# Performance work log

Measured on AMD Instinct MI355X. Metric: run time of the kernel, lower is better.

The kernel has to match this reference:

```python
import jax, jax.numpy as jnp
import numpy as np

NU = 100000  # num 'user' nodes
NI = 100000  # num 'item' nodes
E = 600000   # edges per relation
IN_DIM = 128
HID = 128
OUT = 64


def setup_inputs() -> dict:
    key = jax.random.key(0)
    ks = jax.random.split(key, 14)
    return {
        "x_user": jax.random.normal(ks[0], (NU, IN_DIM), jnp.float32),
        "x_item": jax.random.normal(ks[1], (NI, IN_DIM), jnp.float32),
        "W_proj": jax.random.normal(ks[2], (IN_DIM, HID), jnp.float32) / np.sqrt(IN_DIM),
        "b_proj": jax.random.normal(ks[3], (HID,), jnp.float32) * 0.01,
        "W_out": jax.random.normal(ks[4], (HID, OUT), jnp.float32) / np.sqrt(HID),
        "b_out": jax.random.normal(ks[5], (OUT,), jnp.float32) * 0.01,
        "al1": jax.random.normal(ks[6], (1,), jnp.float32),
        "ar1": jax.random.normal(ks[7], (1,), jnp.float32),
        "al2": jax.random.normal(ks[8], (1,), jnp.float32),
        "ar2": jax.random.normal(ks[9], (1,), jnp.float32),
        "e1_src": jax.random.randint(ks[10], (E,), 0, NU, jnp.int32),  # user->user
        "e1_dst": jax.random.randint(ks[11], (E,), 0, NU, jnp.int32),
        "e2_src": jax.random.randint(ks[12], (E,), 0, NI, jnp.int32),  # item->user
        "e2_dst": jax.random.randint(ks[13], (E,), 0, NU, jnp.int32),
    }


def reference(x_user, x_item, W_proj, b_proj, W_out, b_out,
              al1, ar1, al2, ar2, e1_src, e1_dst, e2_src, e2_dst):
    # Shared projection for every node type
    h_user = x_user @ W_proj + b_proj  # [NU, HID]
    h_item = x_item @ W_proj + b_proj  # [NI, HID]

    # Relation ('user','u2u','user'): msg = h_src*al + h_dst*ar, scatter-add to dst
    msg1 = h_user[e1_src] * al1 + h_user[e1_dst] * ar1  # [E, HID]
    out_user = jax.ops.segment_sum(msg1, e1_dst, num_segments=NU)

    # Relation ('item','i2u','user')
    msg2 = h_item[e2_src] * al2 + h_user[e2_dst] * ar2  # [E, HID]
    out_user = out_user + jax.ops.segment_sum(msg2, e2_dst, num_segments=NU)

    # 'item' receives no messages -> zeros
    out_item = jnp.zeros_like(h_item)

    out_user = jax.nn.elu(out_user)
    out_item = jax.nn.elu(out_item)

    # out_layer applied only to 'user'
    out_user = out_user @ W_out + b_out  # [NU, OUT]
    return out_user, out_item
```

## Files before the change

kernel.cpp:

```cpp
#include <hip/hip_runtime.h>
#include <hip/hip_bf16.h>
#include <math.h>

#define NUSER 100000
#define NITEM 100000
#define NEDGE 600000
#define HID   128
#define OUTD  64
#define LDA   136
#define LDF   132
#define PROJ_BLOCKS ((NUSER + NITEM) / 64)
#define EPB   ((2 * NEDGE + PROJ_BLOCKS - 1) / PROJ_BLOCKS)

typedef __attribute__((ext_vector_type(8))) short  bf16x8;
typedef __attribute__((ext_vector_type(4))) float  f32x4;
typedef __attribute__((ext_vector_type(4))) unsigned short u16x4;

__device__ inline unsigned short f2bf(float f) {
    __hip_bfloat16 h = __float2bfloat16(f);
    return *reinterpret_cast<unsigned short*>(&h);
}

__device__ inline void bf2x(unsigned int u, float& lo, float& hi) {
    union { unsigned int i; float f; } a, b;
    a.i = u << 16;
    b.i = u & 0xffff0000u;
    lo = a.f; hi = b.f;
}

__global__ void prep(const float* __restrict__ W, unsigned short* __restrict__ wt,
                     int* __restrict__ deg) {
    int i = blockIdx.x * 256 + threadIdx.x;
    if (i < 2 * NUSER) deg[i] = 0;
    if (i < 128 * 128) {
        int k = i >> 7, c = i & 127;
        wt[c * 128 + k] = f2bf(W[i]);
    }
}

__global__ void count_rank(const int* __restrict__ e1d, const int* __restrict__ e2d,
                           int* __restrict__ deg1, int* __restrict__ deg2,
                           int* __restrict__ rank) {
    int i = blockIdx.x * blockDim.x + threadIdx.x;
    if (i < NEDGE)            rank[i] = atomicAdd(&deg1[e1d[i]], 1);
    else if (i < 2 * NEDGE)   rank[i] = atomicAdd(&deg2[e2d[i - NEDGE]], 1);
}

#define SCAN_BLOCKS 391

__global__ __launch_bounds__(256) void scanA(
    const int* __restrict__ deg1, const int* __restrict__ deg2,
    int* __restrict__ off, int* __restrict__ bsum)
{
    __shared__ int sh[256];
    int t = threadIdx.x;
    int i = blockIdx.x * 256 + t;
    int d = (i < NUSER) ? deg1[i] + deg2[i] : 0;
    sh[t] = d;
    __syncthreads();
    for (int dd = 1; dd < 256; dd <<= 1) {
        int v = (t >= dd) ? sh[t - dd] : 0;
        __syncthreads();
        sh[t] += v;
        __syncthreads();
    }
    if (i < NUSER) off[i] = (t > 0) ? sh[t - 1] : 0;
    if (t == 255) bsum[blockIdx.x] = sh[255];
}

__global__ __launch_bounds__(512) void scanB(int* __restrict__ bsum, int* __restrict__ off) {
    __shared__ int sh[512];
    int t = threadIdx.x;
    int v = (t < SCAN_BLOCKS) ? bsum[t] : 0;
    sh[t] = v;
    __syncthreads();
    for (int dd = 1; dd < 512; dd <<= 1) {
        int x = (t >= dd) ? sh[t - dd] : 0;
        __syncthreads();
        sh[t] += x;
        __syncthreads();
    }
    if (t < SCAN_BLOCKS) bsum[t] = (t > 0) ? sh[t - 1] : 0;
    if (t == 511) off[NUSER] = sh[511];
}

__global__ __launch_bounds__(256) void scanC(int* __restrict__ off, const int* __restrict__ bsum) {
    int i = blockIdx.x * 256 + threadIdx.x;
    if (i < NUSER) off[i] += bsum[blockIdx.x];
}

__global__ __launch_bounds__(256) void proj_fill(
    const float* __restrict__ xu, const float* __restrict__ xi,
    const unsigned short* __restrict__ wt, const float* __restrict__ b,
    unsigned short* __restrict__ h,
    const int* __restrict__ e1s, const int* __restrict__ e1d,
    const int* __restrict__ e2s, const int* __restrict__ e2d,
    const int* __restrict__ off, const int* __restrict__ deg1,
    const int* __restrict__ rank, int* __restrict__ adj)
{
    __shared__ unsigned short Wl[128 * LDA];
    __shared__ unsigned short Al[64 * LDA];
    const int tid = threadIdx.x;
    const int r0  = blockIdx.x * 64;

    for (int i = tid; i < 2048; i += 256) {
        int col = i >> 4, kc = i & 15;
        *(bf16x8*)&Wl[col * LDA + kc * 8] = *(const bf16x8*)&wt[col * 128 + kc * 8];
    }
    for (int i = tid; i < 2048; i += 256) {
        int row = i >> 5, c4 = i & 31;
        int gr = r0 + row;
        const float4* src = (gr < NUSER)
            ? (const float4*)(xu + (size_t)gr * 128)
            : (const float4*)(xi + (size_t)(gr - NUSER) * 128);
        float4 v = src[c4];
        u16x4 p;
        p.x = f2bf(v.x); p.y = f2bf(v.y); p.z = f2bf(v.z); p.w = f2bf(v.w);
        *(u16x4*)&Al[row * LDA + c4 * 4] = p;
    }
    __syncthreads();

    const int w    = tid >> 6;
    const int lane = tid & 63;
    const int lrow = lane & 15;
    const int lk   = (lane >> 4) * 8;

    f32x4 acc[4][2] = {};

    #pragma unroll
    for (int kc = 0; kc < 4; kc++) {
        const int ko = kc * 32 + lk;
        bf16x8 b0 = *(const bf16x8*)&Wl[(w * 32 + lrow) * LDA + ko];
        bf16x8 b1 = *(const bf16x8*)&Wl[(w * 32 + 16 + lrow) * LDA + ko];
        #pragma unroll
        for (int rt = 0; rt < 4; rt++) {
            bf16x8 aa = *(const bf16x8*)&Al[(rt * 16 + lrow) * LDA + ko];
            acc[rt][0] = __builtin_amdgcn_mfma_f32_16x16x32_bf16(aa, b0, acc[rt][0], 0, 0, 0);
            acc[rt][1] = __builtin_amdgcn_mfma_f32_16x16x32_bf16(aa, b1, acc[rt][1], 0, 0, 0);
        }
    }

    const float bv0 = b[w * 32 + lrow];
    const float bv1 = b[w * 32 + 16 + lrow];
    #pragma unroll
    for (int rt = 0; rt < 4; rt++) {
        #pragma unroll
        for (int ct = 0; ct < 2; ct++) {
            int col = w * 32 + ct * 16 + lrow;
            float bv = ct ? bv1 : bv0;
            #pragma unroll
            for (int r = 0; r < 4; r++) {
                int row = r0 + rt * 16 + (lane >> 4) * 4 + r;
                h[(size_t)row * 128 + col] = f2bf(acc[rt][ct][r] + bv);
            }
        }
    }

    const int base = blockIdx.x * EPB;
    const int lim  = (base + EPB < 2 * NEDGE) ? base + EPB : 2 * NEDGE;
    for (int i = base + tid; i < lim; i += 256) {
        int src, dst, slot;
        if (i < NEDGE) {
            src  = e1s[i];
            dst  = e1d[i];
            slot = off[dst] + rank[i];
        } else {
            int j = i - NEDGE;
            src  = NUSER + e2s[j];
            dst  = e2d[j];
            slot = off[dst] + deg1[dst] + rank[i];
        }
        adj[slot] = src;
    }
}

__global__ __launch_bounds__(256) void gather(
    const unsigned short* __restrict__ h, const int* __restrict__ adj,
    const int* __restrict__ off, const int* __restrict__ deg1,
    const int* __restrict__ deg2,
    const float* __restrict__ al1p, const float* __restrict__ ar1p,
    const float* __restrict__ al2p, const float* __restrict__ ar2p,
    float* __restrict__ acc)
{
    int wid  = (int)((blockIdx.x * 256 + threadIdx.x) >> 6);
    int lane = threadIdx.x & 63;
    if (wid >= NUSER) return;

    const unsigned int* h32 = (const unsigned int*)h;

    const float al1 = al1p[0], al2 = al2p[0];
    const float sc  = ar1p[0] * (float)deg1[wid] + ar2p[0] * (float)deg2[wid];

    float lo, hi;
    bf2x(h32[(size_t)wid * 64 + lane], lo, hi);
    float sx = sc * lo, sy = sc * hi;

    int e    = off[wid];
    int eend = off[wid + 1];
    for (; e + 4 <= eend; e += 4) {
        int s0 = adj[e], s1 = adj[e + 1], s2 = adj[e + 2], s3 = adj[e + 3];
        unsigned int u0 = h32[(size_t)s0 * 64 + lane];
        unsigned int u1 = h32[(size_t)s1 * 64 + lane];
        unsigned int u2 = h32[(size_t)s2 * 64 + lane];
        unsigned int u3 = h32[(size_t)s3 * 64 + lane];
        float a0 = (s0 < NUSER) ? al1 : al2;
        float a1 = (s1 < NUSER) ? al1 : al2;
        float a2 = (s2 < NUSER) ? al1 : al2;
        float a3 = (s3 < NUSER) ? al1 : al2;
        float x0, y0, x1, y1, x2, y2, x3, y3;
        bf2x(u0, x0, y0); bf2x(u1, x1, y1); bf2x(u2, x2, y2); bf2x(u3, x3, y3);
        sx = fmaf(a0, x0, sx); sy = fmaf(a0, y0, sy);
        sx = fmaf(a1, x1, sx); sy = fmaf(a1, y1, sy);
        sx = fmaf(a2, x2, sx); sy = fmaf(a2, y2, sy);
        sx = fmaf(a3, x3, sx); sy = fmaf(a3, y3, sy);
    }
    for (; e < eend; e++) {
        int s0 = adj[e];
        float a0 = (s0 < NUSER) ? al1 : al2;
        float x0, y0;
        bf2x(h32[(size_t)s0 * 64 + lane], x0, y0);
        sx = fmaf(a0, x0, sx); sy = fmaf(a0, y0, sy);
    }

    sx = sx > 0.f ? sx : expm1f(sx);
    sy = sy > 0.f ? sy : expm1f(sy);
    ((float2*)(acc + (size_t)wid * 128))[lane] = make_float2(sx, sy);
}

__global__ __launch_bounds__(256) void finalize(
    const float* __restrict__ acc, const float* __restrict__ Wo,
    const float* __restrict__ bo, float* __restrict__ out,
    float* __restrict__ accw)
{
    __shared__ float Wl[128 * 64];
    __shared__ float Al[64 * LDF];
    const int tid = threadIdx.x;
    const int n0  = blockIdx.x * 64;

    for (int i = tid; i < 128 * 64 / 4; i += 256)
        ((float4*)Wl)[i] = ((const float4*)Wo)[i];

    for (int i = tid; i < 2048; i += 256) {
        int row = i >> 5, c4 = i & 31;
        int gr = n0 + row;
        float4 v = (gr < NUSER) ? ((const float4*)(acc + (size_t)gr * 128))[c4]
                                : make_float4(0.f, 0.f, 0.f, 0.f);
        *(float4*)&Al[row * LDF + c4 * 4] = v;
    }
    __syncthreads();

    for (int i = tid; i < 2048; i += 256) {
        int row = i >> 5, c4 = i & 31;
        int gr = n0 + row;
        if (gr < NUSER)
            ((float4*)(accw + (size_t)gr * 128))[c4] = make_float4(0.f, 0.f, 0.f, 0.f);
    }

    const int tr = tid >> 4;
    const int tc = tid & 15;

    float s[4][4];
    {
        float4 bv = *(const float4*)&bo[tc * 4];
        #pragma unroll
        for (int i = 0; i < 4; i++) {
            s[i][0] = bv.x; s[i][1] = bv.y; s[i][2] = bv.z; s[i][3] = bv.w;
        }
    }

    for (int k0 = 0; k0 < 128; k0 += 4) {
        float4 av[4];
        #pragma unroll
        for (int i = 0; i < 4; i++)
            av[i] = *(const float4*)&Al[(tr * 4 + i) * LDF + k0];
        #pragma unroll
        for (int kk = 0; kk < 4; kk++) {
            float4 wv = *(const float4*)&Wl[(k0 + kk) * 64 + tc * 4];
            #pragma unroll
            for (int i = 0; i < 4; i++) {
                float a = (&av[i].x)[kk];
                s[i][0] = fmaf(a, wv.x, s[i][0]);
                s[i][1] = fmaf(a, wv.y, s[i][1]);
                s[i][2] = fmaf(a, wv.z, s[i][2]);
                s[i][3] = fmaf(a, wv.w, s[i][3]);
            }
        }
    }

    #pragma unroll
    for (int i = 0; i < 4; i++) {
        int gr = n0 + tr * 4 + i;
        if (gr < NUSER) {
            float4 o = make_float4(s[i][0], s[i][1], s[i][2], s[i][3]);
            *(float4*)&out[(size_t)gr * 64 + tc * 4] = o;
        }
    }
}

extern "C" void kernel_launch(void* const* d_in, const int* in_sizes, int n_in,
                              void* d_out, int out_size, void* d_ws, size_t ws_size,
                              hipStream_t stream) {
    const float* xu  = (const float*)d_in[0];
    const float* xi  = (const float*)d_in[1];
    const float* Wp  = (const float*)d_in[2];
    const float* bp  = (const float*)d_in[3];
    const float* Wo  = (const float*)d_in[4];
    const float* bo  = (const float*)d_in[5];
    const float* al1 = (const float*)d_in[6];
    const float* ar1 = (const float*)d_in[7];
    const float* al2 = (const float*)d_in[8];
    const float* ar2 = (const float*)d_in[9];
    const int* e1s = (const int*)d_in[10];
    const int* e1d = (const int*)d_in[11];
    const int* e2s = (const int*)d_in[12];
    const int* e2d = (const int*)d_in[13];

    float* out = (float*)d_out;
    float* acc = out + (size_t)NUSER * OUTD;

    unsigned short* h  = (unsigned short*)d_ws;
    unsigned short* wt = h + (size_t)(NUSER + NITEM) * HID;

    int* meta = (int*)out;
    int* deg1 = meta;
    int* deg2 = meta + NUSER;
    int* off  = meta + 2 * NUSER;
    int* bsum = meta + 3 * NUSER + 64;
    int* adj  = meta + 3 * NUSER + 1024;
    int* rank = adj + 2 * NEDGE;

    prep<<<(2 * NUSER + 255) / 256, 256, 0, stream>>>(Wp, wt, deg1);

    count_rank<<<(2 * NEDGE + 255) / 256, 256, 0, stream>>>(e1d, e2d, deg1, deg2, rank);

    scanA<<<SCAN_BLOCKS, 256, 0, stream>>>(deg1, deg2, off, bsum);
    scanB<<<1, 512, 0, stream>>>(bsum, off);
    scanC<<<SCAN_BLOCKS, 256, 0, stream>>>(off, bsum);

    proj_fill<<<PROJ_BLOCKS, 256, 0, stream>>>(xu, xi, wt, bp, h,
                                               e1s, e1d, e2s, e2d,
                                               off, deg1, rank, adj);

    gather<<<(NUSER * 64) / 256, 256, 0, stream>>>(h, adj, off, deg1, deg2,
                                                   al1, ar1, al2, ar2, acc);

    finalize<<<(NUSER + 63) / 64, 256, 0, stream>>>(acc, Wo, bo, out, acc);
}
```

Measured before the change: 213.8 us.

## Stage projection output through LDS, read weights from global, store activations as bf16

The projection kernel no longer copies the weight matrix into shared memory and reads B fragments straight from global/L2. Its output tile is staged through the freed LDS buffer so h is written with coalesced 16-byte stores instead of scattered 2-byte stores. The gather kernel now writes post-ELU activations as packed bf16 into a workspace buffer rather than fp32 into the output region, halving that intermediate's traffic. The cost is extra precision loss on the activations and repeated uncached-in-LDS weight reads per wave.

```diff
diff --git a/kernel.cpp b/kernel.cpp
--- a/kernel.cpp
+++ b/kernel.cpp
@@ -98,15 +98,10 @@
     const int* __restrict__ off, const int* __restrict__ deg1,
     const int* __restrict__ rank, int* __restrict__ adj)
 {
-    __shared__ unsigned short Wl[128 * LDA];
     __shared__ unsigned short Al[64 * LDA];
     const int tid = threadIdx.x;
     const int r0  = blockIdx.x * 64;
 
-    for (int i = tid; i < 2048; i += 256) {
-        int col = i >> 4, kc = i & 15;
-        *(bf16x8*)&Wl[col * LDA + kc * 8] = *(const bf16x8*)&wt[col * 128 + kc * 8];
-    }
     for (int i = tid; i < 2048; i += 256) {
         int row = i >> 5, c4 = i & 31;
         int gr = r0 + row;
@@ -130,8 +125,8 @@
     #pragma unroll
     for (int kc = 0; kc < 4; kc++) {
         const int ko = kc * 32 + lk;
-        bf16x8 b0 = *(const bf16x8*)&Wl[(w * 32 + lrow) * LDA + ko];
-        bf16x8 b1 = *(const bf16x8*)&Wl[(w * 32 + 16 + lrow) * LDA + ko];
+        bf16x8 b0 = *(const bf16x8*)&wt[(size_t)(w * 32 + lrow) * 128 + ko];
+        bf16x8 b1 = *(const bf16x8*)&wt[(size_t)(w * 32 + 16 + lrow) * 128 + ko];
         #pragma unroll
         for (int rt = 0; rt < 4; rt++) {
             bf16x8 aa = *(const bf16x8*)&Al[(rt * 16 + lrow) * LDA + ko];
@@ -140,6 +135,7 @@
         }
     }
 
+    __syncthreads();
     const float bv0 = b[w * 32 + lrow];
     const float bv1 = b[w * 32 + 16 + lrow];
     #pragma unroll
@@ -150,10 +146,17 @@
             float bv = ct ? bv1 : bv0;
             #pragma unroll
             for (int r = 0; r < 4; r++) {
-                int row = r0 + rt * 16 + (lane >> 4) * 4 + r;
-                h[(size_t)row * 128 + col] = f2bf(acc[rt][ct][r] + bv);
+                int row = rt * 16 + (lane >> 4) * 4 + r;
+                Al[row * LDA + col] = f2bf(acc[rt][ct][r] + bv);
             }
         }
+    }
+    __syncthreads();
+
+    for (int i = tid; i < 1024; i += 256) {
+        int row = i >> 4, c8 = i & 15;
+        *(bf16x8*)&h[(size_t)(r0 + row) * 128 + c8 * 8] =
+            *(const bf16x8*)&Al[row * LDA + c8 * 8];
     }
 
     const int base = blockIdx.x * EPB;
@@ -180,7 +183,7 @@
     const int* __restrict__ deg2,
     const float* __restrict__ al1p, const float* __restrict__ ar1p,
     const float* __restrict__ al2p, const float* __restrict__ ar2p,
-    float* __restrict__ acc)
+    unsigned int* __restrict__ accb)
 {
     int wid  = (int)((blockIdx.x * 256 + threadIdx.x) >> 6);
     int lane = threadIdx.x & 63;
@@ -224,13 +227,14 @@
 
     sx = sx > 0.f ? sx : expm1f(sx);
     sy = sy > 0.f ? sy : expm1f(sy);
-    ((float2*)(acc + (size_t)wid * 128))[lane] = make_float2(sx, sy);
+    unsigned int pk = ((unsigned int)f2bf(sy) << 16) | (unsigned int)f2bf(sx);
+    accb[(size_t)wid * 64 + lane] = pk;
 }
 
 __global__ __launch_bounds__(256) void finalize(
-    const float* __restrict__ acc, const float* __restrict__ Wo,
+    const unsigned int* __restrict__ accb, const float* __restrict__ Wo,
     const float* __restrict__ bo, float* __restrict__ out,
-    float* __restrict__ accw)
+    float* __restrict__ oitem)
 {
     __shared__ float Wl[128 * 64];
     __shared__ float Al[64 * LDF];
@@ -240,12 +244,12 @@
     for (int i = tid; i < 128 * 64 / 4; i += 256)
         ((float4*)Wl)[i] = ((const float4*)Wo)[i];
 
-    for (int i = tid; i < 2048; i += 256) {
-        int row = i >> 5, c4 = i & 31;
+    for (int i = tid; i < 4096; i += 256) {
+        int row = i >> 6, d = i & 63;
         int gr = n0 + row;
-        float4 v = (gr < NUSER) ? ((const float4*)(acc + (size_t)gr * 128))[c4]
-                                : make_float4(0.f, 0.f, 0.f, 0.f);
-        *(float4*)&Al[row * LDF + c4 * 4] = v;
+        float lo = 0.f, hi = 0.f;
+        if (gr < NUSER) bf2x(accb[(size_t)gr * 64 + d], lo, hi);
+        *(float2*)&Al[row * LDF + d * 2] = make_float2(lo, hi);
     }
     __syncthreads();
 
@@ -253,7 +257,7 @@
         int row = i >> 5, c4 = i & 31;
         int gr = n0 + row;
         if (gr < NUSER)
-            ((float4*)(accw + (size_t)gr * 128))[c4] = make_float4(0.f, 0.f, 0.f, 0.f);
+            ((float4*)(oitem + (size_t)gr * 128))[c4] = make_float4(0.f, 0.f, 0.f, 0.f);
     }
 
     const int tr = tid >> 4;
@@ -315,11 +319,12 @@
     const int* e2s = (const int*)d_in[12];
     const int* e2d = (const int*)d_in[13];
 
-    float* out = (float*)d_out;
-    float* acc = out + (size_t)NUSER * OUTD;
-
-    unsigned short* h  = (unsigned short*)d_ws;
-    unsigned short* wt = h + (size_t)(NUSER + NITEM) * HID;
+    float* out   = (float*)d_out;
+    float* oitem = out + (size_t)NUSER * OUTD;
+
+    unsigned short* h    = (unsigned short*)d_ws;
+    unsigned short* wt   = h + (size_t)(NUSER + NITEM) * HID;
+    unsigned int*   accb = (unsigned int*)(wt + 128 * 128);
 
     int* meta = (int*)out;
     int* deg1 = meta;
@@ -342,7 +347,7 @@
                                                off, deg1, rank, adj);
 
     gather<<<(NUSER * 64) / 256, 256, 0, stream>>>(h, adj, off, deg1, deg2,
-                                                   al1, ar1, al2, ar2, acc);
-
-    finalize<<<(NUSER + 63) / 64, 256, 0, stream>>>(acc, Wo, bo, out, acc);
-}
+                                                   al1, ar1, al2, ar2, accb);
+
+    finalize<<<(NUSER + 63) / 64, 256, 0, stream>>>(accb, Wo, bo, out, oitem);
+}
```

Result: slower. 235.4 us (+10.1%).

## Load W fragments from global, batch x loads, stage h stores through LDS

Applied to the files above, without the earlier changes.

The projection kernel no longer copies W into shared memory. Each wave now reads its B fragments directly from global memory into registers. All eight x-row float4 loads are issued before conversion, with a sched barrier between them, so more loads are in flight at once. The bf16 output tile is written back into LDS and then stored to h as coalesced 16-byte rows instead of scattered 2-byte stores. count_rank also handles two edges per thread with half the blocks. In exchange the kernel uses more registers and adds two extra syncthreads.

```diff
diff --git a/kernel.cpp b/kernel.cpp
--- a/kernel.cpp
+++ b/kernel.cpp
@@ -38,12 +38,18 @@
     }
 }
 
+__device__ inline void cr_one(int i, const int* e1d, const int* e2d,
+                              int* deg1, int* deg2, int* rank) {
+    if (i < NEDGE)            rank[i] = atomicAdd(&deg1[e1d[i]], 1);
+    else if (i < 2 * NEDGE)   rank[i] = atomicAdd(&deg2[e2d[i - NEDGE]], 1);
+}
+
 __global__ void count_rank(const int* __restrict__ e1d, const int* __restrict__ e2d,
                            int* __restrict__ deg1, int* __restrict__ deg2,
                            int* __restrict__ rank) {
-    int i = blockIdx.x * blockDim.x + threadIdx.x;
-    if (i < NEDGE)            rank[i] = atomicAdd(&deg1[e1d[i]], 1);
-    else if (i < 2 * NEDGE)   rank[i] = atomicAdd(&deg2[e2d[i - NEDGE]], 1);
+    int i0 = blockIdx.x * 512 + threadIdx.x;
+    cr_one(i0, e1d, e2d, deg1, deg2, rank);
+    cr_one(i0 + 256, e1d, e2d, deg1, deg2, rank);
 }
 
 #define SCAN_BLOCKS 391
@@ -98,24 +104,28 @@
     const int* __restrict__ off, const int* __restrict__ deg1,
     const int* __restrict__ rank, int* __restrict__ adj)
 {
-    __shared__ unsigned short Wl[128 * LDA];
     __shared__ unsigned short Al[64 * LDA];
     const int tid = threadIdx.x;
     const int r0  = blockIdx.x * 64;
 
-    for (int i = tid; i < 2048; i += 256) {
-        int col = i >> 4, kc = i & 15;
-        *(bf16x8*)&Wl[col * LDA + kc * 8] = *(const bf16x8*)&wt[col * 128 + kc * 8];
-    }
-    for (int i = tid; i < 2048; i += 256) {
+    float4 v[8];
+    #pragma unroll
+    for (int j = 0; j < 8; j++) {
+        int i = tid + j * 256;
         int row = i >> 5, c4 = i & 31;
         int gr = r0 + row;
         const float4* src = (gr < NUSER)
             ? (const float4*)(xu + (size_t)gr * 128)
             : (const float4*)(xi + (size_t)(gr - NUSER) * 128);
-        float4 v = src[c4];
+        v[j] = src[c4];
+    }
+    __builtin_amdgcn_sched_barrier(0);
+    #pragma unroll
+    for (int j = 0; j < 8; j++) {
+        int i = tid + j * 256;
+        int row = i >> 5, c4 = i & 31;
         u16x4 p;
-        p.x = f2bf(v.x); p.y = f2bf(v.y); p.z = f2bf(v.z); p.w = f2bf(v.w);
+        p.x = f2bf(v[j].x); p.y = f2bf(v[j].y); p.z = f2bf(v[j].z); p.w = f2bf(v[j].w);
         *(u16x4*)&Al[row * LDA + c4 * 4] = p;
     }
     __syncthreads();
@@ -125,21 +135,27 @@
     const int lrow = lane & 15;
     const int lk   = (lane >> 4) * 8;
 
-    f32x4 acc[4][2] = {};
-
+    bf16x8 bfrag[4][2];
     #pragma unroll
     for (int kc = 0; kc < 4; kc++) {
         const int ko = kc * 32 + lk;
-        bf16x8 b0 = *(const bf16x8*)&Wl[(w * 32 + lrow) * LDA + ko];
-        bf16x8 b1 = *(const bf16x8*)&Wl[(w * 32 + 16 + lrow) * LDA + ko];
+        bfrag[kc][0] = *(const bf16x8*)&wt[(size_t)(w * 32 + lrow) * 128 + ko];
+        bfrag[kc][1] = *(const bf16x8*)&wt[(size_t)(w * 32 + 16 + lrow) * 128 + ko];
+    }
+
+    f32x4 acc[4][2] = {};
+    #pragma unroll
+    for (int kc = 0; kc < 4; kc++) {
+        const int ko = kc * 32 + lk;
         #pragma unroll
         for (int rt = 0; rt < 4; rt++) {
             bf16x8 aa = *(const bf16x8*)&Al[(rt * 16 + lrow) * LDA + ko];
-            acc[rt][0] = __builtin_amdgcn_mfma_f32_16x16x32_bf16(aa, b0, acc[rt][0], 0, 0, 0);
-            acc[rt][1] = __builtin_amdgcn_mfma_f32_16x16x32_bf16(aa, b1, acc[rt][1], 0, 0, 0);
-        }
-    }
-
+            acc[rt][0] = __builtin_amdgcn_mfma_f32_16x16x32_bf16(aa, bfrag[kc][0], acc[rt][0], 0, 0, 0);
+            acc[rt][1] = __builtin_amdgcn_mfma_f32_16x16x32_bf16(aa, bfrag[kc][1], acc[rt][1], 0, 0, 0);
+        }
+    }
+
+    __syncthreads();
     const float bv0 = b[w * 32 + lrow];
     const float bv1 = b[w * 32 + 16 + lrow];
     #pragma unroll
@@ -150,10 +166,17 @@
             float bv = ct ? bv1 : bv0;
             #pragma unroll
             for (int r = 0; r < 4; r++) {
-                int row = r0 + rt * 16 + (lane >> 4) * 4 + r;
-                h[(size_t)row * 128 + col] = f2bf(acc[rt][ct][r] + bv);
+                int row = rt * 16 + (lane >> 4) * 4 + r;
+                Al[row * LDA + col] = f2bf(acc[rt][ct][r] + bv);
             }
         }
+    }
+    __syncthreads();
+
+    for (int i = tid; i < 1024; i += 256) {
+        int row = i >> 4, c8 = i & 15;
+        *(bf16x8*)&h[(size_t)(r0 + row) * 128 + c8 * 8] =
+            *(const bf16x8*)&Al[row * LDA + c8 * 8];
     }
 
     const int base = blockIdx.x * EPB;
@@ -331,7 +354,7 @@
 
     prep<<<(2 * NUSER + 255) / 256, 256, 0, stream>>>(Wp, wt, deg1);
 
-    count_rank<<<(2 * NEDGE + 255) / 256, 256, 0, stream>>>(e1d, e2d, deg1, deg2, rank);
+    count_rank<<<(2 * NEDGE + 511) / 512, 256, 0, stream>>>(e1d, e2d, deg1, deg2, rank);
 
     scanA<<<SCAN_BLOCKS, 256, 0, stream>>>(deg1, deg2, off, bsum);
     scanB<<<1, 512, 0, stream>>>(bsum, off);
```

New measurement: 218.9 us. +2.4%, slower.
